# Kernel optimization log

Measured on AMD Instinct MI355X. Metric: run time of the kernel, lower is better.

Reference implementation:

```python
import jax, jax.numpy as jnp
import numpy as np

T = 2048      # total tokens (single prefill sequence)
HID = 2048    # hidden_size
H = 16        # num k-heads == num v-heads
DK = 128      # key head dim
DV = 128      # value head dim
K = 4         # causal conv kernel width
EPS = 1e-6


def setup_inputs() -> dict:
    key = jax.random.key(0)
    ks = jax.random.split(key, 10)
    n = lambda k, shape, sc: (jax.random.normal(k, shape, jnp.float32) * sc)
    return {
        "hidden_states": n(ks[0], (T, HID), 1.0),
        "Wq": n(ks[1], (HID, H * DK), 0.02),
        "Wk": n(ks[2], (HID, H * DK), 0.02),
        "Wv": n(ks[3], (HID, H * DV), 0.02),
        "Wb": n(ks[4], (HID, H), 0.02),
        "conv_wq": n(ks[5], (H * DK, K), 0.5),
        "conv_wk": n(ks[6], (H * DK, K), 0.5),
        "conv_wv": n(ks[7], (H * DV, K), 0.5),
        "o_norm_w": jnp.ones((DV,), jnp.float32),
        "Wo": n(ks[8], (HID, HID), 0.02),
    }


def _causal_conv_silu(x, w):
    # x: [T, D], w: [D, K] depthwise causal conv, then SiLU (matches causal_conv1d_fn)
    xp = jnp.pad(x, ((K - 1, 0), (0, 0)))
    y = sum(xp[j:j + T] * w[:, j] for j in range(K))
    return jax.nn.silu(y)


def _l2norm(x):
    return x * jax.lax.rsqrt(jnp.sum(x * x, axis=-1, keepdims=True) + EPS)


def reference(hidden_states, Wq, Wk, Wv, Wb, conv_wq, conv_wk, conv_wv, o_norm_w, Wo):
    # projections [T, H*D]
    q = _causal_conv_silu(hidden_states @ Wq, conv_wq).reshape(T, H, DK)
    k = _causal_conv_silu(hidden_states @ Wk, conv_wk).reshape(T, H, DK)
    v = _causal_conv_silu(hidden_states @ Wv, conv_wv).reshape(T, H, DV)
    beta = jax.nn.sigmoid(hidden_states @ Wb)  # [T, H]

    # qk l2-norm + scale (FLA chunk_delta_rule defaults)
    q = _l2norm(q) * (DK ** -0.5)
    k = _l2norm(k)

    # delta-rule recurrence: S <- S + beta * k (v - k^T S)
    def step(S, inp):
        q_t, k_t, v_t, b_t = inp            # [H,DK],[H,DK],[H,DV],[H]
        kS = jnp.einsum('hk,hkv->hv', k_t, S)
        delta = b_t[:, None] * (v_t - kS)   # [H, DV]
        S = S + jnp.einsum('hk,hv->hkv', k_t, delta)
        o_t = jnp.einsum('hk,hkv->hv', q_t, S)
        return S, o_t

    S0 = jnp.zeros((H, DK, DV), jnp.float32)
    _, o = jax.lax.scan(step, S0, (q, k, v, beta))  # o: [T, H, DV]

    # per-head RMSNorm on value head dim
    o = o * jax.lax.rsqrt(jnp.mean(o * o, axis=-1, keepdims=True) + EPS) * o_norm_w
    out = o.reshape(T, H * DV) @ Wo
    return out
```

## Files before the change

### kernel.cpp

```cpp
#include <hip/hip_runtime.h>

typedef unsigned short u16;
typedef __attribute__((ext_vector_type(4))) unsigned short u16x4;
typedef __attribute__((ext_vector_type(8))) unsigned short u16x8;
typedef __attribute__((ext_vector_type(8))) short short8;
typedef __attribute__((ext_vector_type(4))) float f32x4;

#define DEVI __device__ __forceinline__

DEVI u16 f2b(float f) {
  union { float f; unsigned u; } x; x.f = f;
  unsigned r = (x.u + 0x7fffu + ((x.u >> 16) & 1u)) >> 16;
  return (u16)r;
}
DEVI float b2f(u16 h) {
  union { unsigned u; float f; } x; x.u = ((unsigned)h) << 16;
  return x.f;
}
DEVI f32x4 mfma_bf16(short8 a, short8 b, f32x4 c) {
  return __builtin_amdgcn_mfma_f32_16x16x32_bf16(a, b, c, 0, 0, 0);
}
DEVI void gl2lds16(const u16* g, u16* l) {
  __builtin_amdgcn_global_load_lds((__attribute__((address_space(1))) void*)g,
                                   (__attribute__((address_space(3))) void*)l,
                                   16, 0, 0);
}
DEVI void barrier_lds() {
  asm volatile("s_waitcnt lgkmcnt(0)\n\ts_barrier" ::: "memory");
}

__global__ void k_cvt(const float* __restrict__ src, u16* __restrict__ dst, int n4,
                      const float* __restrict__ Wb, u16* __restrict__ WbT) {
  int b = blockIdx.x;
  if (b < 4096) {
    int i = b * 256 + threadIdx.x;
    if (i < n4) {
      float4 v = ((const float4*)src)[i];
      u16x4 r; r.x = f2b(v.x); r.y = f2b(v.y); r.z = f2b(v.z); r.w = f2b(v.w);
      ((u16x4*)dst)[i] = r;
    }
  } else {
    int j = (b - 4096) * 256 + threadIdx.x;
    int n = j >> 11, k = j & 2047;
    WbT[j] = f2b(Wb[k * 16 + n]);
  }
}

__global__ __launch_bounds__(256)
void k_transpose4(const float* __restrict__ s0, const float* __restrict__ s1,
                  const float* __restrict__ s2, const float* __restrict__ s3,
                  u16* __restrict__ d0, u16* __restrict__ d1,
                  u16* __restrict__ d2, u16* __restrict__ d3) {
  const int RC = 2048;
  const float* src = (blockIdx.z == 0) ? s0 : (blockIdx.z == 1) ? s1 : (blockIdx.z == 2) ? s2 : s3;
  u16* dst = (blockIdx.z == 0) ? d0 : (blockIdx.z == 1) ? d1 : (blockIdx.z == 2) ? d2 : d3;
  __shared__ u16 tile[64 * 66];
  int bx = blockIdx.x << 6, by = blockIdx.y << 6;
  int x = threadIdx.x & 63, g = threadIdx.x >> 6;
#pragma unroll
  for (int i = 0; i < 16; ++i) {
    int r = (i << 2) + g;
    tile[x * 66 + r] = f2b(src[(size_t)(by + r) * RC + bx + x]);
  }
  __syncthreads();
#pragma unroll
  for (int i = 0; i < 16; ++i) {
    int r = (i << 2) + g;
    dst[(size_t)(bx + r) * RC + by + x] = tile[r * 66 + x];
  }
}


struct StageCtx { size_t go[2]; int lo[2]; };

DEVI void stage_half(const u16* g, const StageCtx& sc, u16* l) {
  gl2lds16(g + sc.go[0], l + sc.lo[0]);
  gl2lds16(g + sc.go[1], l + sc.lo[1]);
}

DEVI void rdA(const u16* h, const int (&aoff)[4][2], short8 (&a)[4][2]) {
#pragma unroll
  for (int m = 0; m < 4; ++m) {
    a[m][0] = *(const short8*)(h + aoff[m][0]);
    a[m][1] = *(const short8*)(h + aoff[m][1]);
  }
}
DEVI void rdB(const u16* h, const int (&boff)[2][2], short8 (&b)[2][2]) {
#pragma unroll
  for (int n = 0; n < 2; ++n) {
    b[n][0] = *(const short8*)(h + boff[n][0]);
    b[n][1] = *(const short8*)(h + boff[n][1]);
  }
}

template <int QA, int QB>
DEVI void mmquad(const short8 (&a)[4][2], const short8 (&b)[2][2], f32x4 (&acc)[8][4]) {
  __builtin_amdgcn_s_setprio(1);
#pragma unroll
  for (int m = 0; m < 4; ++m)
#pragma unroll
    for (int n = 0; n < 2; ++n) {
      acc[(QA << 2) + m][(QB << 1) + n] =
          mfma_bf16(a[m][0], b[n][0], acc[(QA << 2) + m][(QB << 1) + n]);
      acc[(QA << 2) + m][(QB << 1) + n] =
          mfma_bf16(a[m][1], b[n][1], acc[(QA << 2) + m][(QB << 1) + n]);
    }
  __builtin_amdgcn_s_setprio(0);
}

template <int MODE>
DEVI void ktile(u16* lds, int u,
                const u16* gA0, const u16* gA1, const u16* gB0, const u16* gB1,
                const StageCtx& sc,
                const int (&aoff)[4][2], const int (&boff)[2][2],
                short8 (&a0)[4][2], short8 (&a1)[4][2],
                short8 (&b0)[2][2], short8 (&b1)[2][2],
                f32x4 (&acc)[8][4]) {
  const int cs = (u & 1) << 13, ns = ((u + 1) & 1) << 13;
  const u16* A1c = lds + 16384 + cs;
  const u16* B1c = lds + 49152 + cs;
  const size_t uo1 = (size_t)(u + 1) << 6, uo2 = (size_t)(u + 2) << 6;
  __builtin_amdgcn_s_barrier();
  rdB(B1c, boff, b1);
  if constexpr (MODE <= 1) stage_half(gA1 + uo1, sc, lds + 16384 + ns);
  mmquad<0, 0>(a0, b0, acc);
  __builtin_amdgcn_s_barrier();
  rdA(A1c, aoff, a1);
  if constexpr (MODE == 0) stage_half(gA0 + uo2, sc, lds + cs);
  mmquad<0, 1>(a0, b1, acc);
  __builtin_amdgcn_s_barrier();
  if constexpr (MODE == 0) stage_half(gB0 + uo2, sc, lds + 32768 + cs);
  mmquad<1, 0>(a1, b0, acc);
  if constexpr (MODE == 0) asm volatile("s_waitcnt vmcnt(4)" ::: "memory");
  if constexpr (MODE == 1) asm volatile("s_waitcnt vmcnt(0)" ::: "memory");
  __builtin_amdgcn_s_barrier();
  if constexpr (MODE <= 1) {
    rdA(lds + ns, aoff, a0);
    rdB(lds + 32768 + ns, boff, b0);
  }
  if constexpr (MODE == 0) stage_half(gB1 + uo2, sc, lds + 49152 + cs);
  mmquad<1, 1>(a1, b1, acc);
}

__global__ __launch_bounds__(512, 2)
void k_gemm8p(const u16* __restrict__ A, const u16* __restrict__ BT,
              u16* __restrict__ Cb, int N, int K) {
  __shared__ __align__(16) u16 lds[65536];
  const int tid = threadIdx.x, wave = tid >> 6, lane = tid & 63;
  const int wm = wave >> 2, wn = wave & 3;
  const int fr = lane & 15, fq = (lane >> 4) << 4;
  const long bm = (long)blockIdx.y << 8, bn = (long)blockIdx.x << 8;
  const int NT = K >> 6;
  int aoff[4][2], boff[2][2];
#pragma unroll
  for (int m = 0; m < 4; ++m)
#pragma unroll
    for (int ks = 0; ks < 2; ++ks) {
      int row = (wm << 6) + (m << 4) + fr;
      int kb = (ks << 6) + fq;
      aoff[m][ks] = (row << 6) + ((kb ^ ((fr & 7) << 4)) >> 1);
    }
#pragma unroll
  for (int n = 0; n < 2; ++n)
#pragma unroll
    for (int ks = 0; ks < 2; ++ks) {
      int row = (wn << 5) + (n << 4) + fr;
      int kb = (ks << 6) + fq;
      boff[n][ks] = (row << 6) + ((kb ^ ((fr & 7) << 4)) >> 1);
    }
  StageCtx sc;
#pragma unroll
  for (int s = 0; s < 2; ++s) {
    int c = (s << 9) + tid, row = c >> 3;
    int kbs = (((c & 7) << 4) ^ ((row & 7) << 4));
    sc.go[s] = (size_t)row * K + (kbs >> 1);
    sc.lo[s] = ((s << 9) + (tid & ~63)) << 3;
  }
  const u16* gA0 = A + (size_t)bm * K;
  const u16* gA1 = gA0 + (size_t)128 * K;
  const u16* gB0 = BT + (size_t)bn * K;
  const u16* gB1 = gB0 + (size_t)128 * K;
  f32x4 acc[8][4];
#pragma unroll
  for (int i = 0; i < 8; ++i)
#pragma unroll
    for (int j = 0; j < 4; ++j) acc[i][j] = (f32x4){0.f, 0.f, 0.f, 0.f};
  short8 a0[4][2], a1[4][2], b0[2][2], b1[2][2];
  stage_half(gA0, sc, lds + 0);
  stage_half(gA1, sc, lds + 16384);
  stage_half(gB0, sc, lds + 32768);
  stage_half(gB1, sc, lds + 49152);
  stage_half(gA0 + 64, sc, lds + 8192);
  stage_half(gB0 + 64, sc, lds + 32768 + 8192);
  stage_half(gB1 + 64, sc, lds + 49152 + 8192);
  asm volatile("s_waitcnt vmcnt(6)" ::: "memory");
  __builtin_amdgcn_s_barrier();
  rdA(lds + 0, aoff, a0);
  rdB(lds + 32768, boff, b0);
  for (int u = 0; u + 2 < NT; ++u)
    ktile<0>(lds, u, gA0, gA1, gB0, gB1, sc, aoff, boff, a0, a1, b0, b1, acc);
  ktile<1>(lds, NT - 2, gA0, gA1, gB0, gB1, sc, aoff, boff, a0, a1, b0, b1, acc);
  ktile<2>(lds, NT - 1, gA0, gA1, gB0, gB1, sc, aoff, boff, a0, a1, b0, b1, acc);
  const int er = (lane >> 4) << 2, ec = lane & 15;
#pragma unroll
  for (int ai = 0; ai < 8; ++ai) {
    long row0 = bm + ((long)(ai >> 2) << 7) + (wm << 6) + ((ai & 3) << 4) + er;
#pragma unroll
    for (int bj = 0; bj < 4; ++bj) {
      long col = bn + ((long)(bj >> 1) << 7) + (wn << 5) + ((bj & 1) << 4) + ec;
#pragma unroll
      for (int r = 0; r < 4; ++r)
        Cb[(size_t)(row0 + r) * N + col] = f2b(acc[ai][bj][r]);
    }
  }
}

__global__ __launch_bounds__(256, 4)
void k_gemm_wo(const u16* __restrict__ A, const u16* __restrict__ BT,
               float* __restrict__ Cf, int M, int N, int K) {
  __shared__ __align__(16) u16 As[2048];
  __shared__ __align__(16) u16 Bs[2048];
  const int tid = threadIdx.x, wave = tid >> 6, lane = tid & 63;
  const long bm = (long)blockIdx.y << 6, bn = (long)blockIdx.x << 6;
  const int r0 = (wave << 4) + (lane >> 2);
  const int kof = (((lane & 3) ^ ((lane >> 3) & 3)) << 3);
  const u16* gA = A + (bm + r0) * (long)K + kof;
  const u16* gB = BT + (bn + r0) * (long)K + kof;
  u16* lA = As + (wave << 9);
  u16* lB = Bs + (wave << 9);
  const int wr = (wave >> 1) << 5, wc = (wave & 1) << 5;
  const int fr = lane & 15, fq = (lane >> 4) << 3;
  const int fqs = fq ^ (((fr >> 1) & 3) << 3);
  f32x4 acc[2][2];
#pragma unroll
  for (int i = 0; i < 2; ++i)
#pragma unroll
    for (int j = 0; j < 2; ++j) acc[i][j] = (f32x4){0.f, 0.f, 0.f, 0.f};
  for (int k0 = 0; k0 < K; k0 += 32) {
    gl2lds16(gA + k0, lA);
    gl2lds16(gB + k0, lB);
    __syncthreads();
    short8 af[2], bfr[2];
#pragma unroll
    for (int t = 0; t < 2; ++t) {
      af[t]  = *(const short8*)&As[(wr + (t << 4) + fr) * 32 + fqs];
      bfr[t] = *(const short8*)&Bs[(wc + (t << 4) + fr) * 32 + fqs];
    }
#pragma unroll
    for (int i = 0; i < 2; ++i)
#pragma unroll
      for (int j = 0; j < 2; ++j)
        acc[i][j] = mfma_bf16(af[i], bfr[j], acc[i][j]);
    __syncthreads();
  }
  const int er = (lane >> 4) << 2, ec = lane & 15;
#pragma unroll
  for (int i = 0; i < 2; ++i)
#pragma unroll
    for (int j = 0; j < 2; ++j)
#pragma unroll
      for (int r = 0; r < 4; ++r) {
        long row = bm + wr + (i << 4) + er + r;
        long col = bn + wc + (j << 4) + ec;
        Cf[row * N + col] = acc[i][j][r];
      }
}

__global__ __launch_bounds__(256, 4)
void k_beta(const u16* __restrict__ Xb, const u16* __restrict__ WbT,
            float* __restrict__ beta) {
  __shared__ float part[4][256];
  int tid = threadIdx.x, w = tid >> 6, lane = tid & 63;
  int t0 = blockIdx.x << 4;
  int fr = lane & 15, fq = (lane >> 4) << 3;
  const u16* ap = Xb + (size_t)(t0 + fr) * 2048 + (w << 9) + fq;
  const u16* bp = WbT + (size_t)fr * 2048 + (w << 9) + fq;
  f32x4 acc = {0.f, 0.f, 0.f, 0.f};
#pragma unroll
  for (int ks = 0; ks < 16; ++ks)
    acc = mfma_bf16(*(const short8*)(ap + (ks << 5)), *(const short8*)(bp + (ks << 5)), acc);
  int er = (lane >> 4) << 2;
#pragma unroll
  for (int r = 0; r < 4; ++r) part[w][(er + r) * 16 + fr] = acc[r];
  __syncthreads();
  float s = part[0][tid] + part[1][tid] + part[2][tid] + part[3][tid];
  beta[(t0 << 4) + tid] = 1.f / (1.f + __expf(-s));
}

__global__ __launch_bounds__(256, 4)
void k_conv(const u16* __restrict__ qkv,
            const float* __restrict__ cwq, const float* __restrict__ cwk,
            const float* __restrict__ cwv,
            u16* __restrict__ qn, u16* __restrict__ kn, u16* __restrict__ vn) {
  __shared__ __align__(16) u16 xs[67 * 136];
  __shared__ float wf[128 * 4];
  int tt = blockIdx.x, s = blockIdx.y;
  int kind = s >> 4, h = s & 15;
  int t0 = tt << 6;
  int col = (kind << 11) + (h << 7);
  int tid = threadIdx.x;
  const float* cw = (kind == 0) ? cwq : ((kind == 1) ? cwk : cwv);
  if (tid < 128) *(float4*)&wf[tid << 2] = *(const float4*)(cw + (size_t)((h << 7) + tid) * 4);
  for (int i = tid; i < 1072; i += 256) {
    int prow = i >> 4, c8 = (i & 15) << 3;
    int g = t0 - 3 + prow;
    u16x8 v = {0, 0, 0, 0, 0, 0, 0, 0};
    if (g >= 0) v = *(const u16x8*)(qkv + (size_t)g * 6144 + col + c8);
    *(u16x8*)&xs[prow * 136 + c8] = v;
  }
  __syncthreads();
  int t = tid >> 2, dg = tid & 3;
  float y[32];
  float ss = 0.f;
#pragma unroll
  for (int e8 = 0; e8 < 4; ++e8) {
    int d0 = (dg << 5) + (e8 << 3);
    u16x8 a0 = *(const u16x8*)&xs[(t + 0) * 136 + d0];
    u16x8 a1 = *(const u16x8*)&xs[(t + 1) * 136 + d0];
    u16x8 a2 = *(const u16x8*)&xs[(t + 2) * 136 + d0];
    u16x8 a3 = *(const u16x8*)&xs[(t + 3) * 136 + d0];
#pragma unroll
    for (int e = 0; e < 8; ++e) {
      float4 w = *(const float4*)&wf[(d0 + e) << 2];
      float v = b2f(a0[e]) * w.x + b2f(a1[e]) * w.y + b2f(a2[e]) * w.z + b2f(a3[e]) * w.w;
      v = v / (1.f + __expf(-v));
      y[(e8 << 3) + e] = v;
      ss += v * v;
    }
  }
  float sc = 1.f;
  if (kind < 2) {
    ss += __shfl_xor(ss, 1);
    ss += __shfl_xor(ss, 2);
    sc = rsqrtf(ss + 1e-6f);
    if (kind == 0) sc *= 0.08838834764831843f;
  }
  u16* dst = (kind == 0) ? qn : ((kind == 1) ? kn : vn);
  u16* dp = dst + ((size_t)h << 18) + ((size_t)(t0 + t) << 7) + (dg << 5);
#pragma unroll
  for (int e8 = 0; e8 < 4; ++e8) {
    u16x8 p;
#pragma unroll
    for (int e = 0; e < 8; ++e) p[e] = f2b(y[(e8 << 3) + e] * sc);
    *(u16x8*)(dp + (e8 << 3)) = p;
  }
}

__global__ __launch_bounds__(256, 2)
void k_prep(const u16* __restrict__ qn, const u16* __restrict__ kn, const u16* __restrict__ vn,
            const float* __restrict__ beta,
            u16* __restrict__ Gg, u16* __restrict__ Wg,
            u16* __restrict__ KTg, u16* __restrict__ UTg) {
  __shared__ __align__(16) char sm[70912];
  u16*  Kc  = (u16*)sm;
  u16*  Qc  = (u16*)(sm + 17408);
  u16*  Vc  = (u16*)(sm + 34816);
  u16*  KTl = (u16*)(sm + 52224);
  float* AL = (float*)(sm + 52224);
  float* Bl = (float*)(sm + 70656);
  u16*  WR  = Qc;
  int h = blockIdx.x, c = blockIdx.y;
  int tid = threadIdx.x, wave = tid >> 6, lane = tid & 63;
  size_t ch = (size_t)(c * 16 + h);
  const u16* kb = kn + ((size_t)h << 18) + ((size_t)c << 13);
  const u16* qb = qn + ((size_t)h << 18) + ((size_t)c << 13);
  const u16* vb = vn + ((size_t)h << 18) + ((size_t)c << 13);
#pragma unroll
  for (int s = 0; s < 4; ++s) {
    int e = (tid + (s << 8)) << 3;
    int t = e >> 7, d = e & 127;
    *(u16x8*)&Kc[t * 136 + d] = *(const u16x8*)(kb + e);
    *(u16x8*)&Qc[t * 136 + d] = *(const u16x8*)(qb + e);
    *(u16x8*)&Vc[t * 136 + d] = *(const u16x8*)(vb + e);
  }
  if (tid < 64) Bl[tid] = beta[((c << 6) + tid) * 16 + h];
  __syncthreads();
  int fr = lane & 15, fq = (lane >> 4) << 3, q4 = (lane >> 4) << 2;
  int arow = (wave << 4) + fr;
  f32x4 kk[4], qk[4];
#pragma unroll
  for (int ct = 0; ct < 4; ++ct) { kk[ct] = (f32x4){0.f,0.f,0.f,0.f}; qk[ct] = (f32x4){0.f,0.f,0.f,0.f}; }
#pragma unroll
  for (int ks = 0; ks < 4; ++ks) {
    short8 aK = *(const short8*)&Kc[arow * 136 + (ks << 5) + fq];
    short8 aQ = *(const short8*)&Qc[arow * 136 + (ks << 5) + fq];
#pragma unroll
    for (int ct = 0; ct < 4; ++ct) {
      short8 bK = *(const short8*)&Kc[((ct << 4) + fr) * 136 + (ks << 5) + fq];
      kk[ct] = mfma_bf16(aK, bK, kk[ct]);
      qk[ct] = mfma_bf16(aQ, bK, qk[ct]);
    }
  }
#pragma unroll
  for (int ct = 0; ct < 4; ++ct)
#pragma unroll
    for (int r = 0; r < 4; ++r) {
      int i = (wave << 4) + q4 + r, j = (ct << 4) + fr;
      Gg[(ch << 12) + i * 64 + j] = f2b((j <= i) ? qk[ct][r] : 0.f);
    }
  {
    int d = tid & 127, tg = tid >> 7;
#pragma unroll
    for (int it = 0; it < 4; ++it) {
      int t0 = (tg + (it << 1)) << 3;
      u16x8 pk;
#pragma unroll
      for (int j = 0; j < 8; ++j) pk[j] = Kc[(t0 + j) * 136 + d];
      *(u16x8*)&KTl[d * 72 + t0] = pk;
    }
  }
  __syncthreads();
#pragma unroll
  for (int it = 0; it < 4; ++it) {
    int idx = tid + (it << 8);
    int row = idx >> 3, j8 = (idx & 7) << 3;
    *(u16x8*)(KTg + (ch << 13) + (row << 6) + j8) = *(const u16x8*)&KTl[row * 72 + j8];
  }
  __syncthreads();
  {
    float bi[4];
#pragma unroll
    for (int r = 0; r < 4; ++r) bi[r] = Bl[(wave << 4) + q4 + r];
#pragma unroll
    for (int ct = 0; ct < 4; ++ct)
#pragma unroll
      for (int r = 0; r < 4; ++r) {
        int i = (wave << 4) + q4 + r, j = (ct << 4) + fr;
        AL[i * 64 + j] = (j < i) ? bi[r] * kk[ct][r] : 0.f;
      }
  }
  __syncthreads();
  float X[64];
  {
    const u16* colp = (tid < 128) ? (Kc + tid) : (Vc + (tid - 128));
#pragma unroll
    for (int t = 0; t < 64; ++t) X[t] = Bl[t] * b2f(colp[t * 136]);
#pragma unroll
    for (int r = 1; r < 64; ++r) {
      float s = 0.f;
      const float* Ar = &AL[r * 64];
      int r4 = r & ~3;
#pragma unroll
      for (int l = 0; l < 64; l += 4)
        if (l + 4 <= r) {
          float4 a = *(const float4*)(Ar + l);
          s += a.x * X[l] + a.y * X[l + 1] + a.z * X[l + 2] + a.w * X[l + 3];
        }
#pragma unroll
      for (int l = 0; l < 4; ++l)
        if (r4 + l < r) s += Ar[r4 + l] * X[r4 + l];
      X[r] -= s;
    }
  }
  __syncthreads();
  if (tid < 128) {
#pragma unroll
    for (int t = 0; t < 64; ++t) WR[t * 136 + tid] = f2b(X[t]);
  } else {
    int v = tid - 128;
    u16* dstr = UTg + (ch << 13) + (v << 6);
#pragma unroll
    for (int j = 0; j < 8; ++j) {
      u16x8 p;
#pragma unroll
      for (int e = 0; e < 8; ++e) p[e] = f2b(X[(j << 3) + e]);
      *(u16x8*)(dstr + (j << 3)) = p;
    }
  }
  __syncthreads();
#pragma unroll
  for (int it = 0; it < 4; ++it) {
    int idx = tid + (it << 8);
    int row = idx >> 4, j8 = (idx & 15) << 3;
    *(u16x8*)(Wg + (ch << 13) + (row << 7) + j8) = *(const u16x8*)&WR[row * 136 + j8];
  }
}

struct Frags { short8 q[4], w[4], g[2], k[4]; u16x4 u; };

DEVI void load_frags(Frags& f, const u16* qh, const u16* Wg, const u16* Gg,
                     const u16* KTg, const u16* UTg, int c, int h,
                     int trow, int fr, int fq, int q4, int w, int vbase) {
  const u16* qb = qh + ((size_t)((c << 6) + trow + fr) << 7) + fq;
#pragma unroll
  for (int ks = 0; ks < 4; ++ks) f.q[ks] = *(const short8*)(qb + (ks << 5));
  size_t ch = (size_t)(c * 16 + h);
  const u16* wb = Wg + (ch << 13) + ((size_t)(trow + fr) << 7) + fq;
#pragma unroll
  for (int ks = 0; ks < 4; ++ks) f.w[ks] = *(const short8*)(wb + (ks << 5));
  const u16* gb = Gg + (ch << 12) + ((size_t)(trow + fr) << 6) + fq;
#pragma unroll
  for (int ks = 0; ks < 2; ++ks) f.g[ks] = *(const short8*)(gb + (ks << 5));
  const u16* kbp = KTg + (ch << 13) + ((size_t)(w << 5) << 6) + fq;
#pragma unroll
  for (int dt = 0; dt < 2; ++dt)
#pragma unroll
    for (int ks = 0; ks < 2; ++ks)
      f.k[(dt << 1) | ks] = *(const short8*)(kbp + ((size_t)((dt << 4) + fr) << 6) + (ks << 5));
  f.u = *(const u16x4*)(UTg + (ch << 13) + ((size_t)(vbase + fr) << 6) + trow + q4);
}

DEVI void chunk_body(int c, Frags& f, u16* ST, u16* DT, u16* oh,
                     int trow, int fr, int fq, int q4, int w, int vbase,
                     f32x4& S0, f32x4& S1) {
#pragma unroll
  for (int r = 0; r < 4; ++r) {
    ST[(q4 + r) * 136 + (w << 5) + fr] = f2b(S0[r]);
    ST[(q4 + r) * 136 + (w << 5) + 16 + fr] = f2b(S1[r]);
  }
  barrier_lds();
  short8 sf[4];
#pragma unroll
  for (int ks = 0; ks < 4; ++ks) sf[ks] = *(const short8*)&ST[fr * 136 + (ks << 5) + fq];
  f32x4 racc = {0.f,0.f,0.f,0.f}, oacc = {0.f,0.f,0.f,0.f};
#pragma unroll
  for (int ks = 0; ks < 4; ++ks) {
    racc = mfma_bf16(f.w[ks], sf[ks], racc);
    oacc = mfma_bf16(f.q[ks], sf[ks], oacc);
  }
#pragma unroll
  for (int r = 0; r < 4; ++r)
    DT[fr * 72 + trow + q4 + r] = f2b(b2f(f.u[r]) - racc[r]);
  barrier_lds();
  short8 df[2];
#pragma unroll
  for (int ks = 0; ks < 2; ++ks) df[ks] = *(const short8*)&DT[fr * 72 + (ks << 5) + fq];
#pragma unroll
  for (int ks = 0; ks < 2; ++ks) {
    oacc = mfma_bf16(f.g[ks], df[ks], oacc);
    S0 = mfma_bf16(df[ks], f.k[ks], S0);
    S1 = mfma_bf16(df[ks], f.k[2 | ks], S1);
  }
#pragma unroll
  for (int r = 0; r < 4; ++r)
    oh[(size_t)((c << 6) + trow + q4 + r) * 128 + vbase + fr] = f2b(oacc[r]);
}

__global__ __launch_bounds__(256, 1)
void k_delta(const u16* __restrict__ qn, const u16* __restrict__ Wg,
             const u16* __restrict__ Gg, const u16* __restrict__ KTg,
             const u16* __restrict__ UTg, u16* __restrict__ o) {
  __shared__ __align__(16) u16 ST[16 * 136];
  __shared__ __align__(16) u16 DT[16 * 72];
  int bx = blockIdx.x;
  int h = bx & 15, vbase = (bx >> 4) << 4;
  int tid = threadIdx.x, w = tid >> 6, lane = tid & 63;
  int fr = lane & 15, fq = (lane >> 4) << 3, q4 = (lane >> 4) << 2;
  int trow = w << 4;
  const u16* qh = qn + ((size_t)h << 18);
  u16* oh = o + ((size_t)h << 18);
  f32x4 S0 = {0.f,0.f,0.f,0.f}, S1 = {0.f,0.f,0.f,0.f};
  Frags fa, fb;
  load_frags(fa, qh, Wg, Gg, KTg, UTg, 0, h, trow, fr, fq, q4, w, vbase);
  for (int c = 0; c < 32; c += 2) {
    int c1 = c + 1, c2 = (c + 2 < 32) ? c + 2 : 31;
    load_frags(fb, qh, Wg, Gg, KTg, UTg, c1, h, trow, fr, fq, q4, w, vbase);
    chunk_body(c, fa, ST, DT, oh, trow, fr, fq, q4, w, vbase, S0, S1);
    load_frags(fa, qh, Wg, Gg, KTg, UTg, c2, h, trow, fr, fq, q4, w, vbase);
    chunk_body(c1, fb, ST, DT, oh, trow, fr, fq, q4, w, vbase, S0, S1);
  }
}

__global__ __launch_bounds__(256, 4)
void k_onorm(const u16* __restrict__ o, const float* __restrict__ onw,
             u16* __restrict__ onb) {
  __shared__ float wl[128];
  int tt = blockIdx.x, h = blockIdx.y, tid = threadIdx.x;
  if (tid < 128) wl[tid] = onw[tid];
  __syncthreads();
  int t = tid >> 2, dg = tid & 3;
  const u16* src = o + ((size_t)h << 18) + ((size_t)((tt << 6) + t) << 7) + (dg << 5);
  u16x8 a[4];
  float ss = 0.f;
#pragma unroll
  for (int e8 = 0; e8 < 4; ++e8) {
    a[e8] = *(const u16x8*)(src + (e8 << 3));
#pragma unroll
    for (int e = 0; e < 8; ++e) { float x = b2f(a[e8][e]); ss += x * x; }
  }
  ss += __shfl_xor(ss, 1);
  ss += __shfl_xor(ss, 2);
  float inv = rsqrtf(ss * (1.f / 128.f) + 1e-6f);
  u16* dp = onb + ((size_t)((tt << 6) + t) << 11) + (h << 7) + (dg << 5);
#pragma unroll
  for (int e8 = 0; e8 < 4; ++e8) {
    u16x8 p;
#pragma unroll
    for (int e = 0; e < 8; ++e)
      p[e] = f2b(b2f(a[e8][e]) * inv * wl[(dg << 5) + (e8 << 3) + e]);
    *(u16x8*)(dp + (e8 << 3)) = p;
  }
}

extern "C" void kernel_launch(void* const* d_in, const int* in_sizes, int n_in,
                              void* d_out, int out_size, void* d_ws, size_t ws_size,
                              hipStream_t stream) {
  (void)in_sizes; (void)n_in; (void)out_size; (void)ws_size;
  const float* hs  = (const float*)d_in[0];
  const float* Wq  = (const float*)d_in[1];
  const float* Wk  = (const float*)d_in[2];
  const float* Wv  = (const float*)d_in[3];
  const float* Wb  = (const float*)d_in[4];
  const float* cwq = (const float*)d_in[5];
  const float* cwk = (const float*)d_in[6];
  const float* cwv = (const float*)d_in[7];
  const float* onw = (const float*)d_in[8];
  const float* Wo  = (const float*)d_in[9];
  float* out = (float*)d_out;
  char* ws = (char*)d_ws;
  const size_t MB = 1ull << 20;
  u16*  Xb   = (u16*)(ws);
  u16*  WT   = (u16*)(ws + 8  * MB);
  u16*  WoT  = (u16*)(ws + 32 * MB);
  u16*  QKV  = (u16*)(ws + 40 * MB);
  u16*  Wg   = (u16*)(ws + 40 * MB);
  u16*  KTg  = (u16*)(ws + 48 * MB);
  u16*  UTg  = (u16*)(ws + 56 * MB);
  u16*  qn_  = (u16*)(ws + 64 * MB);
  u16*  kn_  = (u16*)(ws + 72 * MB);
  u16*  vn_  = (u16*)(ws + 80 * MB);
  float* beta= (float*)(ws + 88 * MB);
  u16*  WbT  = (u16*)(ws + 88 * MB + 512 * 1024);
  u16*  Gm   = (u16*)(ws + 89 * MB);
  u16*  o_   = (u16*)(ws + 93 * MB);
  u16*  onb  = (u16*)(ws + 109 * MB);

  k_cvt<<<4224, 256, 0, stream>>>(hs, Xb, 2048 * 2048 / 4, Wb, WbT);
  k_transpose4<<<dim3(32, 32, 4), 256, 0, stream>>>(
      Wq, Wk, Wv, Wo, WT, WT + 2048 * 2048, WT + 2 * 2048 * 2048, WoT);
  k_gemm8p<<<dim3(24, 8), 512, 0, stream>>>(Xb, WT, QKV, 6144, 2048);
  k_beta<<<128, 256, 0, stream>>>(Xb, WbT, beta);
  k_conv<<<dim3(32, 48), 256, 0, stream>>>(QKV, cwq, cwk, cwv, qn_, kn_, vn_);
  k_prep<<<dim3(16, 32), 256, 0, stream>>>(qn_, kn_, vn_, beta, Gm, Wg, KTg, UTg);
  k_delta<<<128, 256, 0, stream>>>(qn_, Wg, Gm, KTg, UTg, o_);
  k_onorm<<<dim3(32, 16), 256, 0, stream>>>(o_, onw, onb);
  k_gemm_wo<<<dim3(32, 32), 256, 0, stream>>>(onb, WoT, out, 2048, 2048, 2048);
}
```

Before: 335.3 us.

## Route Wo projection through split-K 256x256 GEMM and restructure ktile pipeline

The small 64x64-tile Wo GEMM is replaced by the large 256x256 8-wave GEMM, templated to write fp32 partials. K is split four ways across blockIdx.z so 256 blocks fill the device, and a new add kernel sums the four partial buffers. The ktile pipeline is also reordered so fragments are loaded into local registers just before each MMA quad, with extra barriers and waitcnts. The intent is better MFMA efficiency for the output projection, at the cost of extra partial-buffer traffic, an added reduction launch, and possibly less load/compute overlap in the QKV GEMM.

New measurement: 346.8 us. 3.4% more time.

```diff
diff --git a/kernel.cpp b/kernel.cpp
--- a/kernel.cpp
+++ b/kernel.cpp
@@ -113,44 +113,54 @@
                 const u16* gA0, const u16* gA1, const u16* gB0, const u16* gB1,
                 const StageCtx& sc,
                 const int (&aoff)[4][2], const int (&boff)[2][2],
-                short8 (&a0)[4][2], short8 (&a1)[4][2],
-                short8 (&b0)[2][2], short8 (&b1)[2][2],
                 f32x4 (&acc)[8][4]) {
   const int cs = (u & 1) << 13, ns = ((u + 1) & 1) << 13;
-  const u16* A1c = lds + 16384 + cs;
-  const u16* B1c = lds + 49152 + cs;
   const size_t uo1 = (size_t)(u + 1) << 6, uo2 = (size_t)(u + 2) << 6;
-  __builtin_amdgcn_s_barrier();
-  rdB(B1c, boff, b1);
+  short8 a0[4][2], a1[4][2], b0[2][2], b1[2][2];
+  rdA(lds + cs, aoff, a0);
+  rdB(lds + 32768 + cs, boff, b0);
   if constexpr (MODE <= 1) stage_half(gA1 + uo1, sc, lds + 16384 + ns);
+  asm volatile("s_waitcnt lgkmcnt(8)" ::: "memory");
+  __builtin_amdgcn_s_barrier();
+  asm volatile("s_waitcnt lgkmcnt(0)" ::: "memory");
+  __builtin_amdgcn_sched_barrier(0);
   mmquad<0, 0>(a0, b0, acc);
   __builtin_amdgcn_s_barrier();
-  rdA(A1c, aoff, a1);
+  rdB(lds + 49152 + cs, boff, b1);
   if constexpr (MODE == 0) stage_half(gA0 + uo2, sc, lds + cs);
+  __builtin_amdgcn_s_barrier();
+  asm volatile("s_waitcnt lgkmcnt(0)" ::: "memory");
+  __builtin_amdgcn_sched_barrier(0);
   mmquad<0, 1>(a0, b1, acc);
   __builtin_amdgcn_s_barrier();
+  rdA(lds + 16384 + cs, aoff, a1);
   if constexpr (MODE == 0) stage_half(gB0 + uo2, sc, lds + 32768 + cs);
+  __builtin_amdgcn_s_barrier();
+  asm volatile("s_waitcnt lgkmcnt(0)" ::: "memory");
+  __builtin_amdgcn_sched_barrier(0);
   mmquad<1, 0>(a1, b0, acc);
-  if constexpr (MODE == 0) asm volatile("s_waitcnt vmcnt(4)" ::: "memory");
+  __builtin_amdgcn_s_barrier();
+  if constexpr (MODE == 0) {
+    stage_half(gB1 + uo2, sc, lds + 49152 + cs);
+    asm volatile("s_waitcnt vmcnt(6)" ::: "memory");
+  }
   if constexpr (MODE == 1) asm volatile("s_waitcnt vmcnt(0)" ::: "memory");
   __builtin_amdgcn_s_barrier();
-  if constexpr (MODE <= 1) {
-    rdA(lds + ns, aoff, a0);
-    rdB(lds + 32768 + ns, boff, b0);
-  }
-  if constexpr (MODE == 0) stage_half(gB1 + uo2, sc, lds + 49152 + cs);
   mmquad<1, 1>(a1, b1, acc);
-}
-
+  __builtin_amdgcn_s_barrier();
+}
+
+template <int FOUT>
 __global__ __launch_bounds__(512, 2)
 void k_gemm8p(const u16* __restrict__ A, const u16* __restrict__ BT,
-              u16* __restrict__ Cb, int N, int K) {
+              u16* __restrict__ Cb, float* __restrict__ Cf,
+              int N, int K, int NT, size_t czstride) {
   __shared__ __align__(16) u16 lds[65536];
   const int tid = threadIdx.x, wave = tid >> 6, lane = tid & 63;
   const int wm = wave >> 2, wn = wave & 3;
   const int fr = lane & 15, fq = (lane >> 4) << 4;
   const long bm = (long)blockIdx.y << 8, bn = (long)blockIdx.x << 8;
-  const int NT = K >> 6;
+  const int kz = blockIdx.z;
   int aoff[4][2], boff[2][2];
 #pragma unroll
   for (int m = 0; m < 4; ++m)
@@ -176,16 +186,16 @@
     sc.go[s] = (size_t)row * K + (kbs >> 1);
     sc.lo[s] = ((s << 9) + (tid & ~63)) << 3;
   }
-  const u16* gA0 = A + (size_t)bm * K;
+  const size_t kbase = (size_t)kz * ((size_t)NT << 6);
+  const u16* gA0 = A + (size_t)bm * K + kbase;
   const u16* gA1 = gA0 + (size_t)128 * K;
-  const u16* gB0 = BT + (size_t)bn * K;
+  const u16* gB0 = BT + (size_t)bn * K + kbase;
   const u16* gB1 = gB0 + (size_t)128 * K;
   f32x4 acc[8][4];
 #pragma unroll
   for (int i = 0; i < 8; ++i)
 #pragma unroll
     for (int j = 0; j < 4; ++j) acc[i][j] = (f32x4){0.f, 0.f, 0.f, 0.f};
-  short8 a0[4][2], a1[4][2], b0[2][2], b1[2][2];
   stage_half(gA0, sc, lds + 0);
   stage_half(gA1, sc, lds + 16384);
   stage_half(gB0, sc, lds + 32768);
@@ -195,13 +205,12 @@
   stage_half(gB1 + 64, sc, lds + 49152 + 8192);
   asm volatile("s_waitcnt vmcnt(6)" ::: "memory");
   __builtin_amdgcn_s_barrier();
-  rdA(lds + 0, aoff, a0);
-  rdB(lds + 32768, boff, b0);
   for (int u = 0; u + 2 < NT; ++u)
-    ktile<0>(lds, u, gA0, gA1, gB0, gB1, sc, aoff, boff, a0, a1, b0, b1, acc);
-  ktile<1>(lds, NT - 2, gA0, gA1, gB0, gB1, sc, aoff, boff, a0, a1, b0, b1, acc);
-  ktile<2>(lds, NT - 1, gA0, gA1, gB0, gB1, sc, aoff, boff, a0, a1, b0, b1, acc);
+    ktile<0>(lds, u, gA0, gA1, gB0, gB1, sc, aoff, boff, acc);
+  ktile<1>(lds, NT - 2, gA0, gA1, gB0, gB1, sc, aoff, boff, acc);
+  ktile<2>(lds, NT - 1, gA0, gA1, gB0, gB1, sc, aoff, boff, acc);
   const int er = (lane >> 4) << 2, ec = lane & 15;
+  float* cf = Cf + (size_t)kz * czstride;
 #pragma unroll
   for (int ai = 0; ai < 8; ++ai) {
     long row0 = bm + ((long)(ai >> 2) << 7) + (wm << 6) + ((ai & 3) << 4) + er;
@@ -209,61 +218,25 @@
     for (int bj = 0; bj < 4; ++bj) {
       long col = bn + ((long)(bj >> 1) << 7) + (wn << 5) + ((bj & 1) << 4) + ec;
 #pragma unroll
-      for (int r = 0; r < 4; ++r)
-        Cb[(size_t)(row0 + r) * N + col] = f2b(acc[ai][bj][r]);
-    }
-  }
-}
-
-__global__ __launch_bounds__(256, 4)
-void k_gemm_wo(const u16* __restrict__ A, const u16* __restrict__ BT,
-               float* __restrict__ Cf, int M, int N, int K) {
-  __shared__ __align__(16) u16 As[2048];
-  __shared__ __align__(16) u16 Bs[2048];
-  const int tid = threadIdx.x, wave = tid >> 6, lane = tid & 63;
-  const long bm = (long)blockIdx.y << 6, bn = (long)blockIdx.x << 6;
-  const int r0 = (wave << 4) + (lane >> 2);
-  const int kof = (((lane & 3) ^ ((lane >> 3) & 3)) << 3);
-  const u16* gA = A + (bm + r0) * (long)K + kof;
-  const u16* gB = BT + (bn + r0) * (long)K + kof;
-  u16* lA = As + (wave << 9);
-  u16* lB = Bs + (wave << 9);
-  const int wr = (wave >> 1) << 5, wc = (wave & 1) << 5;
-  const int fr = lane & 15, fq = (lane >> 4) << 3;
-  const int fqs = fq ^ (((fr >> 1) & 3) << 3);
-  f32x4 acc[2][2];
-#pragma unroll
-  for (int i = 0; i < 2; ++i)
-#pragma unroll
-    for (int j = 0; j < 2; ++j) acc[i][j] = (f32x4){0.f, 0.f, 0.f, 0.f};
-  for (int k0 = 0; k0 < K; k0 += 32) {
-    gl2lds16(gA + k0, lA);
-    gl2lds16(gB + k0, lB);
-    __syncthreads();
-    short8 af[2], bfr[2];
-#pragma unroll
-    for (int t = 0; t < 2; ++t) {
-      af[t]  = *(const short8*)&As[(wr + (t << 4) + fr) * 32 + fqs];
-      bfr[t] = *(const short8*)&Bs[(wc + (t << 4) + fr) * 32 + fqs];
-    }
-#pragma unroll
-    for (int i = 0; i < 2; ++i)
-#pragma unroll
-      for (int j = 0; j < 2; ++j)
-        acc[i][j] = mfma_bf16(af[i], bfr[j], acc[i][j]);
-    __syncthreads();
-  }
-  const int er = (lane >> 4) << 2, ec = lane & 15;
-#pragma unroll
-  for (int i = 0; i < 2; ++i)
-#pragma unroll
-    for (int j = 0; j < 2; ++j)
-#pragma unroll
       for (int r = 0; r < 4; ++r) {
-        long row = bm + wr + (i << 4) + er + r;
-        long col = bn + wc + (j << 4) + ec;
-        Cf[row * N + col] = acc[i][j][r];
+        if (FOUT) cf[(size_t)(row0 + r) * N + col] = acc[ai][bj][r];
+        else      Cb[(size_t)(row0 + r) * N + col] = f2b(acc[ai][bj][r]);
       }
+    }
+  }
+}
+
+__global__ __launch_bounds__(256)
+void k_add4(const float* __restrict__ p, float* __restrict__ out, size_t stride4) {
+  size_t i = (size_t)blockIdx.x * 256 + threadIdx.x;
+  const float4* p4 = (const float4*)p;
+  float4 a = p4[i], b = p4[i + stride4], c = p4[i + 2 * stride4], d = p4[i + 3 * stride4];
+  float4 r;
+  r.x = (a.x + b.x) + (c.x + d.x);
+  r.y = (a.y + b.y) + (c.y + d.y);
+  r.z = (a.z + b.z) + (c.z + d.z);
+  r.w = (a.w + b.w) + (c.w + d.w);
+  ((float4*)out)[i] = r;
 }
 
 __global__ __launch_bounds__(256, 4)
@@ -624,15 +597,18 @@
   u16*  Gm   = (u16*)(ws + 89 * MB);
   u16*  o_   = (u16*)(ws + 93 * MB);
   u16*  onb  = (u16*)(ws + 109 * MB);
+  float* Pk  = (float*)(ws + 40 * MB);
 
   k_cvt<<<4224, 256, 0, stream>>>(hs, Xb, 2048 * 2048 / 4, Wb, WbT);
   k_transpose4<<<dim3(32, 32, 4), 256, 0, stream>>>(
       Wq, Wk, Wv, Wo, WT, WT + 2048 * 2048, WT + 2 * 2048 * 2048, WoT);
-  k_gemm8p<<<dim3(24, 8), 512, 0, stream>>>(Xb, WT, QKV, 6144, 2048);
+  k_gemm8p<0><<<dim3(24, 8, 1), 512, 0, stream>>>(Xb, WT, QKV, nullptr, 6144, 2048, 32, 0);
   k_beta<<<128, 256, 0, stream>>>(Xb, WbT, beta);
   k_conv<<<dim3(32, 48), 256, 0, stream>>>(QKV, cwq, cwk, cwv, qn_, kn_, vn_);
   k_prep<<<dim3(16, 32), 256, 0, stream>>>(qn_, kn_, vn_, beta, Gm, Wg, KTg, UTg);
   k_delta<<<128, 256, 0, stream>>>(qn_, Wg, Gm, KTg, UTg, o_);
   k_onorm<<<dim3(32, 16), 256, 0, stream>>>(o_, onw, onb);
-  k_gemm_wo<<<dim3(32, 32), 256, 0, stream>>>(onb, WoT, out, 2048, 2048, 2048);
-}
+  k_gemm8p<1><<<dim3(8, 8, 4), 512, 0, stream>>>(onb, WoT, nullptr, Pk, 2048, 2048, 8,
+                                                 (size_t)2048 * 2048);
+  k_add4<<<4096, 256, 0, stream>>>(Pk, out, (size_t)2048 * 2048 / 4);
+}
```
